# Optimization experiments

Measured on AMD Instinct MI355X. Metric: run time of the kernel, lower is better.

Reference implementation:

```python
import jax, jax.numpy as jnp
import numpy as np

B, L, D, H = 4, 256, 256, 8
DH = D // H


def setup_inputs() -> dict:
    key = jax.random.key(0)
    ks = jax.random.split(key, 12)
    s = 1.0 / np.sqrt(D)
    return {
        "inputs": jax.random.normal(ks[0], (B, L, D), jnp.float32),
        "mask": jax.random.bernoulli(ks[1], 0.15, (B, L, L)),
        "rel_emb": jax.random.normal(ks[2], (B, L, L, D), jnp.float32) * 0.05,
        "Wq": jax.random.normal(ks[3], (D, D), jnp.float32) * s,
        "bq": jnp.zeros((D,), jnp.float32),
        "Wk": jax.random.normal(ks[4], (D, D), jnp.float32) * s,
        "bk": jnp.zeros((D,), jnp.float32),
        "Wv": jax.random.normal(ks[5], (D, D), jnp.float32) * s,
        "bv": jnp.zeros((D,), jnp.float32),
        "Wo": jax.random.normal(ks[6], (D, D), jnp.float32) * s,
        "bo": jnp.zeros((D,), jnp.float32),
        "u": jax.random.normal(ks[7], (D,), jnp.float32),
        "v_param": jax.random.normal(ks[8], (D,), jnp.float32),
    }


def _shape(x):
    # (B, L, D) -> (B, H, L, DH)
    return x.reshape(B, L, H, DH).transpose(0, 2, 1, 3)


def reference(inputs, mask, rel_emb, Wq, bq, Wk, bk, Wv, bv, Wo, bo, u, v_param):
    q = _shape(inputs @ Wq.T + bq) / np.sqrt(DH)  # (B,H,L,DH), pre-scaled
    k = _shape(inputs @ Wk.T + bk)
    val = _shape(inputs @ Wv.T + bv)

    u_h = u.reshape(1, H, 1, DH)
    v_h = v_param.reshape(1, H, 1, DH)

    # content term: (q+u) k^T
    a_c = jnp.einsum('bhqd,bhkd->bhqk', q + u_h, k)
    # position term: (q+v) rel_emb^T, rel_emb per (q,k) pair
    rel = rel_emb.reshape(B, L, L, H, DH)
    b_d = jnp.einsum('bhqd,bqkhd->bhqk', q + v_h, rel)

    scores = (a_c + b_d).astype(jnp.float32)
    scores = jnp.where(mask[:, None, :, :], -1e18, scores)
    attn = jax.nn.softmax(scores, axis=-1)  # (B,H,L,L)

    ctx = jnp.einsum('bhqk,bhkd->bhqd', attn, val)
    ctx = ctx.transpose(0, 2, 1, 3).reshape(B, L, D)
    out = ctx @ Wo.T + bo
    return (out, attn)
```

## Files before the change

kernel.cpp:

```cpp
#include <hip/hip_runtime.h>
#include <hip/hip_bf16.h>

#define BB  4
#define LL  256
#define DD  256
#define HH  8
#define DHH 32
#define BL  1024

__global__ __launch_bounds__(1024) void mask_detect_kernel(
    const unsigned int* __restrict__ w, unsigned int* __restrict__ flags) {
  __shared__ int sf32, shib;
  const int t = threadIdx.x;
  if (t == 0) { sf32 = 0; shib = 0; }
  __syncthreads();
  int f = 0, hb = 0;
  for (int i = t; i < 16384; i += 1024) {
    unsigned int x = w[i];
    if (x == 0x3F800000u) f = 1;
    else if (x & 0xFFFFFF00u) hb = 1;
  }
  if (f)  atomicOr(&sf32, 1);
  if (hb) atomicOr(&shib, 1);
  __syncthreads();
  if (t == 0) flags[0] = (sf32 || !shib) ? 1u : 0u;
}

__global__ __launch_bounds__(256) void qkv_kernel(
    const float* __restrict__ X,
    const float* __restrict__ Wq, const float* __restrict__ bq,
    const float* __restrict__ Wk, const float* __restrict__ bk,
    const float* __restrict__ Wv, const float* __restrict__ bv,
    const float* __restrict__ u,  const float* __restrict__ vp,
    float* __restrict__ qu, float* __restrict__ qv,
    float* __restrict__ K,  float* __restrict__ V) {
  const int row0 = blockIdx.x * 4;
  const int c = threadIdx.x;
  float accq[4] = {0.f, 0.f, 0.f, 0.f};
  float acck[4] = {0.f, 0.f, 0.f, 0.f};
  float accv[4] = {0.f, 0.f, 0.f, 0.f};
  const float4* Wq4 = (const float4*)(Wq + c * DD);
  const float4* Wk4 = (const float4*)(Wk + c * DD);
  const float4* Wv4 = (const float4*)(Wv + c * DD);
  const float4* X4  = (const float4*)X;
  const int xbase = row0 * (DD / 4);
#pragma unroll 8
  for (int j4 = 0; j4 < DD / 4; ++j4) {
    const float4 wq = Wq4[j4], wk = Wk4[j4], wv = Wv4[j4];
#pragma unroll
    for (int r = 0; r < 4; ++r) {
      const float4 x = X4[xbase + r * (DD / 4) + j4];
      accq[r] += x.x * wq.x + x.y * wq.y + x.z * wq.z + x.w * wq.w;
      acck[r] += x.x * wk.x + x.y * wk.y + x.z * wk.z + x.w * wk.w;
      accv[r] += x.x * wv.x + x.y * wv.y + x.z * wv.z + x.w * wv.w;
    }
  }
  const float scale = 0.17677669529663687f;
  const float uc = u[c], vc = vp[c], bqc = bq[c], bkc = bk[c], bvc = bv[c];
#pragma unroll
  for (int r = 0; r < 4; ++r) {
    const int idx = (row0 + r) * DD + c;
    const float pq = (accq[r] + bqc) * scale;
    qu[idx] = pq + uc;
    qv[idx] = pq + vc;
    K[idx]  = acck[r] + bkc;
    V[idx]  = accv[r] + bvc;
  }
}

__global__ __launch_bounds__(512, 8) void attn_kernel(
    const float* __restrict__ qu, const float* __restrict__ qv,
    const float* __restrict__ Km, const float* __restrict__ Vm,
    const float* __restrict__ rel, const void* __restrict__ mask_raw,
    const unsigned int* __restrict__ flags,
    float* __restrict__ attn_out, float* __restrict__ ctx) {
  const int bq = blockIdx.x;
  const int b = bq >> 8, q = bq & 255;
  const int t = threadIdx.x;
  const int wave = t >> 6, lane = t & 63;
  __shared__ float qu_s[DD], qv_s[DD];
  __shared__ float msk_s[LL];
  __shared__ float sc[HH][LL + 4];
  __shared__ float pctx[HH][DD + 4];

  if (t < 256) {
    qu_s[t] = qu[bq * DD + t];
    qv_s[t] = qv[bq * DD + t];
    bool masked;
    if (flags[0]) masked = ((const unsigned int*)mask_raw)[bq * LL + t] != 0u;
    else          masked = ((const unsigned char*)mask_raw)[bq * LL + t] != 0;
    msk_s[t] = masked ? 1.f : 0.f;
  }
  __syncthreads();

  const float4 u4 = ((const float4*)qu_s)[lane];
  const float4 w4 = ((const float4*)qv_s)[lane];
  const int h_of_lane = lane >> 3;
  const int k0 = wave * 32;
  const float4* K4 = (const float4*)(Km + (size_t)b * LL * DD) +
                     (size_t)k0 * 64 + lane;
  const float4* R4 = (const float4*)(rel + (size_t)bq * LL * DD) +
                     (size_t)k0 * 64 + lane;
#pragma unroll 4
  for (int i = 0; i < 32; ++i) {
    const int k = k0 + i;
    const float4 kk = K4[(size_t)i * 64];
    const float4 rr = R4[(size_t)i * 64];
    float s = u4.x * kk.x + u4.y * kk.y + u4.z * kk.z + u4.w * kk.w
            + w4.x * rr.x + w4.y * rr.y + w4.z * rr.z + w4.w * rr.w;
    s += __shfl_xor(s, 1);
    s += __shfl_xor(s, 2);
    s += __shfl_xor(s, 4);
    if ((lane & 7) == 0)
      sc[h_of_lane][k] = (msk_s[k] != 0.f) ? -1e18f : s;
  }
  __syncthreads();

  {
    const int h = wave;
    float v0 = sc[h][lane], v1 = sc[h][lane + 64];
    float v2 = sc[h][lane + 128], v3 = sc[h][lane + 192];
    float m = fmaxf(fmaxf(v0, v1), fmaxf(v2, v3));
#pragma unroll
    for (int off = 32; off >= 1; off >>= 1) m = fmaxf(m, __shfl_xor(m, off));
    float e0 = __expf(v0 - m), e1 = __expf(v1 - m);
    float e2 = __expf(v2 - m), e3 = __expf(v3 - m);
    float s = (e0 + e1) + (e2 + e3);
#pragma unroll
    for (int off = 32; off >= 1; off >>= 1) s += __shfl_xor(s, off);
    const float inv = 1.0f / s;
    e0 *= inv; e1 *= inv; e2 *= inv; e3 *= inv;
    sc[h][lane] = e0; sc[h][lane + 64] = e1;
    sc[h][lane + 128] = e2; sc[h][lane + 192] = e3;
    float* aout = attn_out + (((size_t)(b * HH + h) * LL + q) * LL);
    aout[lane] = e0; aout[lane + 64] = e1;
    aout[lane + 128] = e2; aout[lane + 192] = e3;
  }
  __syncthreads();

  {
    const float4* V4 = (const float4*)(Vm + (size_t)b * LL * DD) +
                       (size_t)k0 * 64 + lane;
    float4 acc = make_float4(0.f, 0.f, 0.f, 0.f);
#pragma unroll 4
    for (int i = 0; i < 32; ++i) {
      const float a = sc[h_of_lane][k0 + i];
      const float4 vv = V4[(size_t)i * 64];
      acc.x += a * vv.x; acc.y += a * vv.y;
      acc.z += a * vv.z; acc.w += a * vv.w;
    }
    ((float4*)&pctx[wave][0])[lane] = acc;
  }
  __syncthreads();

  if (t < 256) {
    float s = 0.f;
#pragma unroll
    for (int w = 0; w < HH; ++w) s += pctx[w][t];
    ctx[bq * DD + t] = s;
  }
}

__global__ __launch_bounds__(256) void outproj_kernel(
    const float* __restrict__ ctx, const float* __restrict__ Wo,
    const float* __restrict__ bo, float* __restrict__ out) {
  const int row0 = blockIdx.x * 4;
  const int c = threadIdx.x;
  float acc[4] = {0.f, 0.f, 0.f, 0.f};
  const float4* W4 = (const float4*)(Wo + c * DD);
  const float4* X4 = (const float4*)ctx;
  const int xbase = row0 * (DD / 4);
#pragma unroll 8
  for (int j4 = 0; j4 < DD / 4; ++j4) {
    const float4 w = W4[j4];
#pragma unroll
    for (int r = 0; r < 4; ++r) {
      const float4 x = X4[xbase + r * (DD / 4) + j4];
      acc[r] += x.x * w.x + x.y * w.y + x.z * w.z + x.w * w.w;
    }
  }
  const float boc = bo[c];
#pragma unroll
  for (int r = 0; r < 4; ++r) out[(row0 + r) * DD + c] = acc[r] + boc;
}

extern "C" void kernel_launch(void* const* d_in, const int* in_sizes, int n_in,
                              void* d_out, int out_size, void* d_ws, size_t ws_size,
                              hipStream_t stream) {
  (void)in_sizes; (void)n_in; (void)out_size; (void)ws_size;
  const float* X   = (const float*)d_in[0];
  const void*  msk = d_in[1];
  const float* rel = (const float*)d_in[2];
  const float* Wq  = (const float*)d_in[3];
  const float* bq  = (const float*)d_in[4];
  const float* Wk  = (const float*)d_in[5];
  const float* bk  = (const float*)d_in[6];
  const float* Wv  = (const float*)d_in[7];
  const float* bv  = (const float*)d_in[8];
  const float* Wo  = (const float*)d_in[9];
  const float* bo  = (const float*)d_in[10];
  const float* u   = (const float*)d_in[11];
  const float* vp  = (const float*)d_in[12];

  float* out  = (float*)d_out;
  float* attn = out + BL * DD;

  float* ws_f = (float*)d_ws;
  float* qu  = ws_f;
  float* qv  = qu + BL * DD;
  float* K   = qv + BL * DD;
  float* V   = K  + BL * DD;
  float* ctx = V  + BL * DD;
  unsigned int* flags = (unsigned int*)(ctx + BL * DD);

  mask_detect_kernel<<<1, 1024, 0, stream>>>((const unsigned int*)msk, flags);
  qkv_kernel<<<BL / 4, 256, 0, stream>>>(X, Wq, bq, Wk, bk, Wv, bv, u, vp,
                                         qu, qv, K, V);
  attn_kernel<<<BL, 512, 0, stream>>>(qu, qv, K, V, rel, msk, flags, attn, ctx);
  outproj_kernel<<<BL / 4, 256, 0, stream>>>(ctx, Wo, bo, out);
}
```

Measured before the change: 113.1 us.

## Process two queries per attention block and fold mask detection into QKV kernel

The attention kernel now handles two query rows per block, so each K and V row loaded from global memory serves both queries. This halves the block count and doubles shared-memory use, and launch bounds drop from 8 to 4 blocks per CU. The mask-format detection kernel becomes an extra block of the QKV projection launch, which removes one kernel launch. The rel_emb stream, the dominant traffic, is unchanged, so the gain depends on K/V reuse and launch overhead.

```diff
diff --git a/kernel.cpp b/kernel.cpp
--- a/kernel.cpp
+++ b/kernel.cpp
@@ -8,34 +8,35 @@
 #define DHH 32
 #define BL  1024
 
-__global__ __launch_bounds__(1024) void mask_detect_kernel(
-    const unsigned int* __restrict__ w, unsigned int* __restrict__ flags) {
-  __shared__ int sf32, shib;
-  const int t = threadIdx.x;
-  if (t == 0) { sf32 = 0; shib = 0; }
-  __syncthreads();
-  int f = 0, hb = 0;
-  for (int i = t; i < 16384; i += 1024) {
-    unsigned int x = w[i];
-    if (x == 0x3F800000u) f = 1;
-    else if (x & 0xFFFFFF00u) hb = 1;
-  }
-  if (f)  atomicOr(&sf32, 1);
-  if (hb) atomicOr(&shib, 1);
-  __syncthreads();
-  if (t == 0) flags[0] = (sf32 || !shib) ? 1u : 0u;
-}
-
 __global__ __launch_bounds__(256) void qkv_kernel(
     const float* __restrict__ X,
     const float* __restrict__ Wq, const float* __restrict__ bq,
     const float* __restrict__ Wk, const float* __restrict__ bk,
     const float* __restrict__ Wv, const float* __restrict__ bv,
     const float* __restrict__ u,  const float* __restrict__ vp,
+    const unsigned int* __restrict__ mask_w,
     float* __restrict__ qu, float* __restrict__ qv,
-    float* __restrict__ K,  float* __restrict__ V) {
+    float* __restrict__ K,  float* __restrict__ V,
+    unsigned int* __restrict__ flags) {
+  const int t = threadIdx.x;
+  if (blockIdx.x == 256) {
+    __shared__ int sf32, shib;
+    if (t == 0) { sf32 = 0; shib = 0; }
+    __syncthreads();
+    int f = 0, hb = 0;
+    for (int i = t; i < 16384; i += 256) {
+      unsigned int x = mask_w[i];
+      if (x == 0x3F800000u) f = 1;
+      else if (x & 0xFFFFFF00u) hb = 1;
+    }
+    if (f)  atomicOr(&sf32, 1);
+    if (hb) atomicOr(&shib, 1);
+    __syncthreads();
+    if (t == 0) flags[0] = (sf32 || !shib) ? 1u : 0u;
+    return;
+  }
   const int row0 = blockIdx.x * 4;
-  const int c = threadIdx.x;
+  const int c = t;
   float accq[4] = {0.f, 0.f, 0.f, 0.f};
   float acck[4] = {0.f, 0.f, 0.f, 0.f};
   float accv[4] = {0.f, 0.f, 0.f, 0.f};
@@ -68,58 +69,70 @@
   }
 }
 
-__global__ __launch_bounds__(512, 8) void attn_kernel(
+__global__ __launch_bounds__(512, 4) void attn_kernel(
     const float* __restrict__ qu, const float* __restrict__ qv,
     const float* __restrict__ Km, const float* __restrict__ Vm,
     const float* __restrict__ rel, const void* __restrict__ mask_raw,
     const unsigned int* __restrict__ flags,
     float* __restrict__ attn_out, float* __restrict__ ctx) {
-  const int bq = blockIdx.x;
-  const int b = bq >> 8, q = bq & 255;
+  const int blk = blockIdx.x;
+  const int b = blk >> 7;
+  const int q0 = (blk & 127) * 2;
   const int t = threadIdx.x;
   const int wave = t >> 6, lane = t & 63;
-  __shared__ float qu_s[DD], qv_s[DD];
-  __shared__ float msk_s[LL];
-  __shared__ float sc[HH][LL + 4];
-  __shared__ float pctx[HH][DD + 4];
-
-  if (t < 256) {
-    qu_s[t] = qu[bq * DD + t];
-    qv_s[t] = qv[bq * DD + t];
+  __shared__ float qu_s[2][DD], qv_s[2][DD];
+  __shared__ float msk_s[2][LL];
+  __shared__ float sc[2][HH][LL + 4];
+  __shared__ float pctx[2][HH][DD + 4];
+
+  {
+    const int qq = t >> 8, d = t & 255;
+    const int bq = b * LL + q0 + qq;
+    qu_s[qq][d] = qu[bq * DD + d];
+    qv_s[qq][d] = qv[bq * DD + d];
     bool masked;
-    if (flags[0]) masked = ((const unsigned int*)mask_raw)[bq * LL + t] != 0u;
-    else          masked = ((const unsigned char*)mask_raw)[bq * LL + t] != 0;
-    msk_s[t] = masked ? 1.f : 0.f;
-  }
-  __syncthreads();
-
-  const float4 u4 = ((const float4*)qu_s)[lane];
-  const float4 w4 = ((const float4*)qv_s)[lane];
-  const int h_of_lane = lane >> 3;
+    if (flags[0]) masked = ((const unsigned int*)mask_raw)[bq * LL + d] != 0u;
+    else          masked = ((const unsigned char*)mask_raw)[bq * LL + d] != 0;
+    msk_s[qq][d] = masked ? 1.f : 0.f;
+  }
+  __syncthreads();
+
+  const float4 u40 = ((const float4*)qu_s[0])[lane];
+  const float4 u41 = ((const float4*)qu_s[1])[lane];
+  const float4 w40 = ((const float4*)qv_s[0])[lane];
+  const float4 w41 = ((const float4*)qv_s[1])[lane];
+  const int hol = lane >> 3;
   const int k0 = wave * 32;
-  const float4* K4 = (const float4*)(Km + (size_t)b * LL * DD) +
-                     (size_t)k0 * 64 + lane;
-  const float4* R4 = (const float4*)(rel + (size_t)bq * LL * DD) +
-                     (size_t)k0 * 64 + lane;
+  const float4* K4  = (const float4*)(Km + (size_t)b * LL * DD) +
+                      (size_t)k0 * 64 + lane;
+  const float4* R40 = (const float4*)rel +
+                      (size_t)(b * LL + q0) * (LL * 64) + (size_t)k0 * 64 + lane;
+  const float4* R41 = R40 + (size_t)LL * 64;
 #pragma unroll 4
   for (int i = 0; i < 32; ++i) {
     const int k = k0 + i;
     const float4 kk = K4[(size_t)i * 64];
-    const float4 rr = R4[(size_t)i * 64];
-    float s = u4.x * kk.x + u4.y * kk.y + u4.z * kk.z + u4.w * kk.w
-            + w4.x * rr.x + w4.y * rr.y + w4.z * rr.z + w4.w * rr.w;
-    s += __shfl_xor(s, 1);
-    s += __shfl_xor(s, 2);
-    s += __shfl_xor(s, 4);
-    if ((lane & 7) == 0)
-      sc[h_of_lane][k] = (msk_s[k] != 0.f) ? -1e18f : s;
-  }
-  __syncthreads();
-
-  {
-    const int h = wave;
-    float v0 = sc[h][lane], v1 = sc[h][lane + 64];
-    float v2 = sc[h][lane + 128], v3 = sc[h][lane + 192];
+    const float4 r0 = R40[(size_t)i * 64];
+    const float4 r1 = R41[(size_t)i * 64];
+    float s0 = u40.x * kk.x + u40.y * kk.y + u40.z * kk.z + u40.w * kk.w
+             + w40.x * r0.x + w40.y * r0.y + w40.z * r0.z + w40.w * r0.w;
+    float s1 = u41.x * kk.x + u41.y * kk.y + u41.z * kk.z + u41.w * kk.w
+             + w41.x * r1.x + w41.y * r1.y + w41.z * r1.z + w41.w * r1.w;
+    s0 += __shfl_xor(s0, 1); s0 += __shfl_xor(s0, 2); s0 += __shfl_xor(s0, 4);
+    s1 += __shfl_xor(s1, 1); s1 += __shfl_xor(s1, 2); s1 += __shfl_xor(s1, 4);
+    if ((lane & 7) == 0) {
+      sc[0][hol][k] = (msk_s[0][k] != 0.f) ? -1e18f : s0;
+      sc[1][hol][k] = (msk_s[1][k] != 0.f) ? -1e18f : s1;
+    }
+  }
+  __syncthreads();
+
+#pragma unroll
+  for (int pp = 0; pp < 2; ++pp) {
+    const int pair = wave + pp * 8;
+    const int qq = pair >> 3, h = pair & 7;
+    float v0 = sc[qq][h][lane], v1 = sc[qq][h][lane + 64];
+    float v2 = sc[qq][h][lane + 128], v3 = sc[qq][h][lane + 192];
     float m = fmaxf(fmaxf(v0, v1), fmaxf(v2, v3));
 #pragma unroll
     for (int off = 32; off >= 1; off >>= 1) m = fmaxf(m, __shfl_xor(m, off));
@@ -130,9 +143,9 @@
     for (int off = 32; off >= 1; off >>= 1) s += __shfl_xor(s, off);
     const float inv = 1.0f / s;
     e0 *= inv; e1 *= inv; e2 *= inv; e3 *= inv;
-    sc[h][lane] = e0; sc[h][lane + 64] = e1;
-    sc[h][lane + 128] = e2; sc[h][lane + 192] = e3;
-    float* aout = attn_out + (((size_t)(b * HH + h) * LL + q) * LL);
+    sc[qq][h][lane] = e0; sc[qq][h][lane + 64] = e1;
+    sc[qq][h][lane + 128] = e2; sc[qq][h][lane + 192] = e3;
+    float* aout = attn_out + (((size_t)(b * HH + h) * LL + (q0 + qq)) * LL);
     aout[lane] = e0; aout[lane + 64] = e1;
     aout[lane + 128] = e2; aout[lane + 192] = e3;
   }
@@ -141,23 +154,28 @@
   {
     const float4* V4 = (const float4*)(Vm + (size_t)b * LL * DD) +
                        (size_t)k0 * 64 + lane;
-    float4 acc = make_float4(0.f, 0.f, 0.f, 0.f);
+    float4 a0 = make_float4(0.f, 0.f, 0.f, 0.f);
+    float4 a1 = make_float4(0.f, 0.f, 0.f, 0.f);
 #pragma unroll 4
     for (int i = 0; i < 32; ++i) {
-      const float a = sc[h_of_lane][k0 + i];
+      const int k = k0 + i;
+      const float p0 = sc[0][hol][k];
+      const float p1 = sc[1][hol][k];
       const float4 vv = V4[(size_t)i * 64];
-      acc.x += a * vv.x; acc.y += a * vv.y;
-      acc.z += a * vv.z; acc.w += a * vv.w;
-    }
-    ((float4*)&pctx[wave][0])[lane] = acc;
-  }
-  __syncthreads();
-
-  if (t < 256) {
+      a0.x += p0 * vv.x; a0.y += p0 * vv.y; a0.z += p0 * vv.z; a0.w += p0 * vv.w;
+      a1.x += p1 * vv.x; a1.y += p1 * vv.y; a1.z += p1 * vv.z; a1.w += p1 * vv.w;
+    }
+    ((float4*)&pctx[0][wave][0])[lane] = a0;
+    ((float4*)&pctx[1][wave][0])[lane] = a1;
+  }
+  __syncthreads();
+
+  {
+    const int qq = t >> 8, d = t & 255;
     float s = 0.f;
 #pragma unroll
-    for (int w = 0; w < HH; ++w) s += pctx[w][t];
-    ctx[bq * DD + t] = s;
+    for (int w = 0; w < HH; ++w) s += pctx[qq][w][d];
+    ctx[(size_t)(b * LL + q0 + qq) * DD + d] = s;
   }
 }
 
@@ -213,9 +231,10 @@
   float* ctx = V  + BL * DD;
   unsigned int* flags = (unsigned int*)(ctx + BL * DD);
 
-  mask_detect_kernel<<<1, 1024, 0, stream>>>((const unsigned int*)msk, flags);
-  qkv_kernel<<<BL / 4, 256, 0, stream>>>(X, Wq, bq, Wk, bk, Wv, bv, u, vp,
-                                         qu, qv, K, V);
-  attn_kernel<<<BL, 512, 0, stream>>>(qu, qv, K, V, rel, msk, flags, attn, ctx);
+  qkv_kernel<<<257, 256, 0, stream>>>(X, Wq, bq, Wk, bk, Wv, bv, u, vp,
+                                      (const unsigned int*)msk,
+                                      qu, qv, K, V, flags);
+  attn_kernel<<<BL / 2, 512, 0, stream>>>(qu, qv, K, V, rel, msk, flags,
+                                          attn, ctx);
   outproj_kernel<<<BL / 4, 256, 0, stream>>>(ctx, Wo, bo, out);
 }
```

Result: faster. 105.8 us (-6.5%).
